# Kernel tuning notes

Measured on AMD Instinct MI355X. Metric: run time of the kernel, lower is better.

Reference implementation:

```python
import jax, jax.numpy as jnp
import numpy as np

N_NODES = 50000
N_EDGES = 800000
D_IN = 128
D_HID = 128
GN_EPS = 1e-5
L2_EPS = 1e-12


def _gcn_conv(x, edge_index, W, b, num_nodes):
    """PyG GCNConv: symmetric normalization with self-loops; x [N, Fin]."""
    src, dst = edge_index[0], edge_index[1]
    loops = jnp.arange(num_nodes, dtype=src.dtype)
    src = jnp.concatenate([src, loops])
    dst = jnp.concatenate([dst, loops])
    ew = jnp.ones(src.shape[0], dtype=x.dtype)
    deg = jax.ops.segment_sum(ew, dst, num_segments=num_nodes)
    dinv = jnp.where(deg > 0, jax.lax.rsqrt(deg), 0.0)
    norm = dinv[src] * dinv[dst]                       # [E+N]
    xw = x @ W                                         # [N, Fout]
    msg = xw[src] * norm[:, None]                      # gather + scale
    out = jax.ops.segment_sum(msg, dst, num_segments=num_nodes)
    return out + b


def _message_norm(x, msg, scale):
    """PyG MessageNorm(learn_scale=True): x + scale * ||x|| * msg/||msg||."""
    msg_n = msg / jnp.maximum(jnp.linalg.norm(msg, axis=-1, keepdims=True), L2_EPS)
    x_norm = jnp.linalg.norm(x, axis=-1, keepdims=True)
    return x + scale * x_norm * msg_n


def _graph_norm(x, weight, bias, mean_scale):
    """PyG GraphNorm, single graph (batch all zeros)."""
    mean = jnp.mean(x, axis=0, keepdims=True)
    out = x - mean * mean_scale
    var = jnp.mean(out * out, axis=0, keepdims=True)
    return weight * out * jax.lax.rsqrt(var + GN_EPS) + bias


def _gelu(x):
    return jax.nn.gelu(x, approximate=False)


def setup_inputs() -> dict:
    key = jax.random.key(0)
    ks = jax.random.split(key, 4)
    X = jax.random.normal(ks[0], (D_IN, N_NODES), dtype=jnp.float32)
    edge_index = jax.random.randint(ks[1], (2, N_EDGES), 0, N_NODES, dtype=jnp.int64)
    W1 = jax.random.normal(ks[2], (D_IN, D_HID), dtype=jnp.float32) * (1.0 / np.sqrt(D_IN))
    b1 = jnp.zeros((D_HID,), dtype=jnp.float32)
    scale1 = jnp.ones((1,), dtype=jnp.float32)
    W2 = jax.random.normal(ks[3], (D_HID, D_IN), dtype=jnp.float32) * (1.0 / np.sqrt(D_HID))
    b2 = jnp.zeros((D_IN,), dtype=jnp.float32)
    scale2 = jnp.ones((1,), dtype=jnp.float32)
    gn_weight = jnp.ones((D_IN,), dtype=jnp.float32)
    gn_bias = jnp.zeros((D_IN,), dtype=jnp.float32)
    gn_mean_scale = jnp.ones((D_IN,), dtype=jnp.float32)
    return {"X": X, "edge_index": edge_index, "W1": W1, "b1": b1, "scale1": scale1,
            "W2": W2, "b2": b2, "scale2": scale2, "gn_weight": gn_weight,
            "gn_bias": gn_bias, "gn_mean_scale": gn_mean_scale}


def reference(X, edge_index, W1, b1, scale1, W2, b2, scale2,
              gn_weight, gn_bias, gn_mean_scale):
    x = X.T                                            # [N, D_IN]
    n = x.shape[0]
    # GCNChain 1
    f = _gelu(_message_norm(x, _gcn_conv(x, edge_index, W1, b1, n), scale1))
    # GCNChain 2
    f = _gelu(_message_norm(f, _gcn_conv(f, edge_index, W2, b2, n), scale2))
    # residual + GraphNorm + GELU
    return _gelu(_graph_norm(f + x, gn_weight, gn_bias, gn_mean_scale))
```

## Files before the change

### kernel.cpp

```cpp
#include <hip/hip_runtime.h>
#include <math.h>

#define D 128
#define CAP 64
#define NBUCK 56
#define BSZ   894
#define CAPB  15360

typedef _Float16 h8 __attribute__((ext_vector_type(8)));
typedef float f4x __attribute__((ext_vector_type(4)));

__device__ __forceinline__ float gelu_f(float v){
    return 0.5f * v * (1.0f + erff(v * 0.70710678f));
}

__global__ void k_init(int* cnt, float* colsum, float* colsq, int* gcur,
                       const float* __restrict__ W1, const float* __restrict__ W2,
                       _Float16* __restrict__ wz1, _Float16* __restrict__ wz2, int N){
    int i = blockIdx.x*blockDim.x + threadIdx.x;
    if (i < N) cnt[i] = 0;
    if (i < D){ colsum[i] = 0.f; colsq[i] = 0.f; }
    if (i < NBUCK) gcur[i] = 0;
    if (i < 32768){
        const float* W = (i < 16384) ? W1 : W2;
        _Float16* wz   = (i < 16384) ? wz1 : wz2;
        int u = i & 16383;
        int jj = u & 7, l = (u>>3)&63, fi = u>>9;
        int kb = fi>>3, j = fi&7;
        int k = kb*32 + (l>>4)*8 + jj;
        int c = j*16 + (l&15);
        wz[u] = (_Float16)W[k*D + c];
    }
}

__global__ __launch_bounds__(256)
void k_part(const int* __restrict__ ei, int* __restrict__ gcur,
            unsigned int* __restrict__ ebin, int E){
    __shared__ int bcnt[NBUCK], bbase[NBUCK], bcur[NBUCK];
    int t = threadIdx.x;
    int chunk = (E + gridDim.x - 1) / gridDim.x;
    int e0 = blockIdx.x*chunk, e1 = min(e0 + chunk, E);
    if (t < NBUCK){ bcnt[t] = 0; bcur[t] = 0; }
    __syncthreads();
    int sl[13], dl[13];
    #pragma unroll
    for (int k = 0; k < 13; k++){
        int e = e0 + t + k*256;
        sl[k] = -1;
        if (e < e1){
            sl[k] = __builtin_nontemporal_load(&ei[e]);
            dl[k] = __builtin_nontemporal_load(&ei[E + e]);
            atomicAdd(&bcnt[dl[k]/BSZ], 1);
        }
    }
    __syncthreads();
    if (t < NBUCK) bbase[t] = atomicAdd(&gcur[t], bcnt[t]);
    __syncthreads();
    #pragma unroll
    for (int k = 0; k < 13; k++){
        if (sl[k] >= 0){
            int d = dl[k], b = d/BSZ;
            int p = atomicAdd(&bcur[b], 1);
            int idx = bbase[b] + p;
            if (idx < CAPB)
                ebin[(size_t)b*CAPB + idx] = ((unsigned)(d - b*BSZ) << 16) | (unsigned)sl[k];
        }
    }
}

__global__ __launch_bounds__(256)
void k_fill2(const unsigned int* __restrict__ ebin, const int* __restrict__ gcur,
             int* cnt, unsigned short* __restrict__ csrc){
    int j = blockIdx.x;
    int x = j & 7, i = j >> 3;
    int b = x*7 + (i % 7);
    int slice = i / 7;
    int cntb = gcur[b]; if (cntb > CAPB) cntb = CAPB;
    int chunk = (cntb + 13) / 14;
    int st = slice*chunk, en = min(st + chunk, cntb);
    const unsigned int* bp = ebin + (size_t)b*CAPB;
    for (int e = st + threadIdx.x; e < en; e += 256){
        unsigned pk = bp[e];
        int s = pk & 0xFFFF;
        int d = b*BSZ + (int)(pk >> 16);
        int p = atomicAdd(&cnt[d], 1);
        if (p < CAP) csrc[(size_t)d*CAP + p] = (unsigned short)s;
    }
}

template<bool TRANS_IN>
__launch_bounds__(256)
__global__ void k_gemm_mfma(const void* __restrict__ inp, const h8* __restrict__ wz,
                            const int* __restrict__ cnt, _Float16* __restrict__ outh,
                            h8* __restrict__ xt16, int N){
    __shared__ _Float16 a_lds[8192];
    int t = threadIdx.x;
    int n0 = blockIdx.x * 64;

    if (TRANS_IN){
        const float* in = (const float*)inp;
        #pragma unroll
        for (int i = 0; i < 32; i++){
            int idx = i*256 + t;
            int k = idx >> 6, nn = idx & 63;
            int n = n0 + nn;
            float v = (n < N) ? in[(size_t)k*N + n] : 0.f;
            int kb = k>>5, ks = k&31;
            int lane = (ks>>3)*16 + (nn&15);
            int w = nn>>4;
            a_lds[((kb*4 + w)*64 + lane)*8 + (ks&7)] = (_Float16)v;
        }
    } else {
        const h8* in = (const h8*)inp;
        #pragma unroll
        for (int i = 0; i < 4; i++){
            int idx8 = i*256 + t;
            int nn = idx8 >> 4, kq = idx8 & 15;
            int n = n0 + nn;
            h8 v = {};
            if (n < N) v = in[(size_t)n*16 + kq];
            int kb = kq>>2, quad = kq&3;
            int lane = quad*16 + (nn&15);
            int w = nn>>4;
            *(h8*)&a_lds[((kb*4 + w)*64 + lane)*8] = v;
        }
    }
    __syncthreads();

    int w = t>>6, l = t&63;
    f4x acc[8];
    #pragma unroll
    for (int j = 0; j < 8; j++) acc[j] = (f4x){0.f, 0.f, 0.f, 0.f};
    #pragma unroll
    for (int kb = 0; kb < 4; kb++){
        h8 a = *(const h8*)&a_lds[((kb*4 + w)*64 + l)*8];
        #pragma unroll
        for (int j = 0; j < 8; j++){
            h8 b = wz[(kb*8 + j)*64 + l];
            acc[j] = __builtin_amdgcn_mfma_f32_16x16x32_f16(a, b, acc[j], 0, 0, 0);
        }
    }

    int quad = l>>4, m = l&15;
    #pragma unroll
    for (int r = 0; r < 4; r++){
        int node = n0 + w*16 + quad*4 + r;
        if (node < N){
            float dv = rsqrtf((float)(cnt[node] + 1));
            #pragma unroll
            for (int j = 0; j < 8; j++)
                outh[(size_t)node*D + j*16 + m] = (_Float16)(acc[j][r] * dv);
        }
    }

    if (TRANS_IN && xt16){
        int node = t>>2, kb = t&3;
        int n = n0 + node;
        if (n < N){
            #pragma unroll
            for (int q = 0; q < 4; q++){
                h8 v = *(const h8*)&a_lds[((kb*4 + (node>>4))*64 + q*16 + (node&15))*8];
                xt16[(size_t)n*16 + kb*4 + q] = v;
            }
        }
    }
}

template<bool FINAL>
__launch_bounds__(256)
__global__ void k_gather(const h8* __restrict__ y, const h8* __restrict__ resid,
                         const h8* __restrict__ xorig,
                         const int* __restrict__ cnt,
                         const unsigned short* __restrict__ csrc,
                         const float* __restrict__ bias,
                         const float* __restrict__ scale,
                         h8* __restrict__ out16, int N){
    int n = blockIdx.x*16 + (threadIdx.x >> 4);
    if (n >= N) return;
    int lane = threadIdx.x & 15;
    h8 a0 = y[(size_t)n*16 + lane];
    h8 a1 = {0,0,0,0,0,0,0,0};
    h8 a2 = {0,0,0,0,0,0,0,0};
    h8 a3 = {0,0,0,0,0,0,0,0};
    int mraw = cnt[n];
    float dv = rsqrtf((float)(mraw + 1));
    int m = (mraw < CAP) ? mraw : CAP;
    const unsigned short* sp = csrc + (size_t)n*CAP;
    int j = 0;
    for (; j + 8 <= m; j += 8){
        int s0 = sp[j+0], s1 = sp[j+1], s2 = sp[j+2], s3 = sp[j+3];
        int s4 = sp[j+4], s5 = sp[j+5], s6 = sp[j+6], s7 = sp[j+7];
        h8 v0 = y[(size_t)s0*16 + lane];
        h8 v1 = y[(size_t)s1*16 + lane];
        h8 v2 = y[(size_t)s2*16 + lane];
        h8 v3 = y[(size_t)s3*16 + lane];
        h8 v4 = y[(size_t)s4*16 + lane];
        h8 v5 = y[(size_t)s5*16 + lane];
        h8 v6 = y[(size_t)s6*16 + lane];
        h8 v7 = y[(size_t)s7*16 + lane];
        a0 += v0; a1 += v1; a2 += v2; a3 += v3;
        a0 += v4; a1 += v5; a2 += v6; a3 += v7;
    }
    for (; j + 4 <= m; j += 4){
        int s0 = sp[j+0], s1 = sp[j+1], s2 = sp[j+2], s3 = sp[j+3];
        h8 v0 = y[(size_t)s0*16 + lane];
        h8 v1 = y[(size_t)s1*16 + lane];
        h8 v2 = y[(size_t)s2*16 + lane];
        h8 v3 = y[(size_t)s3*16 + lane];
        a0 += v0; a1 += v1; a2 += v2; a3 += v3;
    }
    for (; j < m; j++){
        int s0 = sp[j];
        a1 += y[(size_t)s0*16 + lane];
    }
    h8 ah = (a0 + a1) + (a2 + a3);

    const float4* bp = (const float4*)&bias[lane*8];
    float4 b0 = bp[0], b1 = bp[1];
    float c[8];
    float nc = 0.f;
    #pragma unroll
    for (int i = 0; i < 8; i++){
        float bb = (i < 4) ? (&b0.x)[i] : (&b1.x)[i-4];
        c[i] = bb + dv * (float)ah[i];
        nc += c[i]*c[i];
    }
    h8 rv = resid[(size_t)n*16 + lane];
    float r[8];
    float nr = 0.f;
    #pragma unroll
    for (int i = 0; i < 8; i++){ r[i] = (float)rv[i]; nr += r[i]*r[i]; }
    #pragma unroll
    for (int mm = 8; mm > 0; mm >>= 1){
        nc += __shfl_xor(nc, mm, 64);
        nr += __shfl_xor(nr, mm, 64);
    }
    float sc = scale[0] * sqrtf(nr) / fmaxf(sqrtf(nc), 1e-12f);
    h8 o;
    #pragma unroll
    for (int i = 0; i < 8; i++){
        float g = gelu_f(r[i] + sc*c[i]);
        if (FINAL){
            h8 xv = xorig[(size_t)n*16 + lane];
            g += (float)xv[i];
        }
        o[i] = (_Float16)g;
    }
    out16[(size_t)n*16 + lane] = o;
}

__global__ void k_stats(const _Float16* __restrict__ h, float* colsum, float* colsq, int N){
    __shared__ float ls[256], ls2[256];
    int t = threadIdx.x;
    int f = t & 127, half = t >> 7;
    float s = 0.f, s2 = 0.f;
    for (int n = blockIdx.x*2 + half; n < N; n += gridDim.x*2){
        float v = (float)h[(size_t)n*D + f]; s += v; s2 += v*v;
    }
    ls[t] = s; ls2[t] = s2;
    __syncthreads();
    if (t < 128){
        s  = ls[t]  + ls[t+128];
        s2 = ls2[t] + ls2[t+128];
        atomicAdd(&colsum[f], s);
        atomicAdd(&colsq[f], s2);
    }
}

__global__ void k_final(const h8* __restrict__ h16,
                        const float* __restrict__ colsum, const float* __restrict__ colsq,
                        const float* __restrict__ gw, const float* __restrict__ gb,
                        const float* __restrict__ ms,
                        float* __restrict__ outp, int N){
    __shared__ float cf[D], sh[D];
    int t = threadIdx.x;
    if (t < D){
        float invN = 1.0f / (float)N;
        float mean = colsum[t] * invN;
        float c = mean * ms[t];
        float var = colsq[t]*invN - 2.f*c*mean + c*c;
        float a = gw[t] * rsqrtf(var + 1e-5f);
        cf[t] = a;
        sh[t] = gb[t] - c*a;
    }
    __syncthreads();
    int i = blockIdx.x*blockDim.x + t;
    if (i < N*16){
        int n = i >> 4, lane = i & 15;
        h8 v = h16[i];
        int f = lane*8;
        float4 o0, o1;
        o0.x = gelu_f((float)v[0]*cf[f+0] + sh[f+0]);
        o0.y = gelu_f((float)v[1]*cf[f+1] + sh[f+1]);
        o0.z = gelu_f((float)v[2]*cf[f+2] + sh[f+2]);
        o0.w = gelu_f((float)v[3]*cf[f+3] + sh[f+3]);
        o1.x = gelu_f((float)v[4]*cf[f+4] + sh[f+4]);
        o1.y = gelu_f((float)v[5]*cf[f+5] + sh[f+5]);
        o1.z = gelu_f((float)v[6]*cf[f+6] + sh[f+6]);
        o1.w = gelu_f((float)v[7]*cf[f+7] + sh[f+7]);
        *(float4*)&outp[(size_t)n*D + f]     = o0;
        *(float4*)&outp[(size_t)n*D + f + 4] = o1;
    }
}

extern "C" void kernel_launch(void* const* d_in, const int* in_sizes, int n_in,
                              void* d_out, int out_size, void* d_ws, size_t ws_size,
                              hipStream_t stream){
    const float* X   = (const float*)d_in[0];
    const int*   ei  = (const int*)  d_in[1];
    const float* W1  = (const float*)d_in[2];
    const float* b1  = (const float*)d_in[3];
    const float* s1  = (const float*)d_in[4];
    const float* W2  = (const float*)d_in[5];
    const float* b2  = (const float*)d_in[6];
    const float* s2  = (const float*)d_in[7];
    const float* gw  = (const float*)d_in[8];
    const float* gb  = (const float*)d_in[9];
    const float* gms = (const float*)d_in[10];
    int N = in_sizes[0] / D;
    int E = in_sizes[1] / 2;
    float* out = (float*)d_out;

    char* ws = (char*)d_ws;
    size_t o = 0;
    auto alloc = [&](size_t bytes)->void*{
        o = (o + 255) & ~(size_t)255;
        void* p = ws + o; o += bytes; return p;
    };
    int*            cnt    = (int*)           alloc((size_t)N * sizeof(int));
    unsigned short* csrc   = (unsigned short*)alloc((size_t)N * CAP * sizeof(unsigned short));
    unsigned int*   ebin   = (unsigned int*)  alloc((size_t)NBUCK * CAPB * sizeof(unsigned int));
    int*            gcur   = (int*)           alloc(NBUCK * sizeof(int));
    float*          colsum = (float*)         alloc(D * sizeof(float));
    float*          colsq  = (float*)         alloc(D * sizeof(float));
    _Float16*       wz1    = (_Float16*)      alloc(16384 * sizeof(_Float16));
    _Float16*       wz2    = (_Float16*)      alloc(16384 * sizeof(_Float16));
    _Float16*       A      = (_Float16*)      alloc((size_t)N * D * sizeof(_Float16));
    h8*             XT16   = (h8*)            alloc((size_t)N * D * sizeof(_Float16));
    h8*             F1     = (h8*)            alloc((size_t)N * D * sizeof(_Float16));
    h8*             B16    = (h8*)            alloc((size_t)N * D * sizeof(_Float16));

    k_init<<<(N+255)/256, 256, 0, stream>>>(cnt, colsum, colsq, gcur, W1, W2, wz1, wz2, N);
    k_part<<<256, 256, 0, stream>>>(ei, gcur, ebin, E);
    k_fill2<<<784, 256, 0, stream>>>(ebin, gcur, cnt, csrc);

    k_gemm_mfma<true><<<(N+63)/64, 256, 0, stream>>>(X, (const h8*)wz1, cnt, A, XT16, N);
    k_gather<false><<<(N+15)/16, 256, 0, stream>>>((const h8*)A, XT16, (const h8*)nullptr,
                                                   cnt, csrc, b1, s1, F1, N);
    k_gemm_mfma<false><<<(N+63)/64, 256, 0, stream>>>(F1, (const h8*)wz2, cnt, A, (h8*)nullptr, N);
    k_gather<true><<<(N+15)/16, 256, 0, stream>>>((const h8*)A, F1, XT16,
                                                  cnt, csrc, b2, s2, B16, N);
    k_stats<<<256, 256, 0, stream>>>((const _Float16*)B16, colsum, colsq, N);
    k_final<<<(N*16+255)/256, 256, 0, stream>>>(B16, colsum, colsq, gw, gb, gms, out, N);
}
```

Baseline: 276.6 us.

## Build CSR per bucket in LDS and fuse first gather with second GEMM

Destination buckets become power-of-two sized (512 nodes). k_fill2 now builds each bucket's neighbour lists and counts in shared memory, then copies them to global memory in coalesced form. This removes the global atomics on cnt and the separate zeroing of cnt. The first aggregation + MessageNorm + GELU is fused with the second MFMA GEMM, so F1 no longer has to be read back from global memory, and one launch is dropped. In exchange, the fill step runs on only 98 large blocks each using about 66KB of LDS, and the fused gather uses 4x fewer, longer-running blocks, which may hide gather latency less well.

```diff
diff --git a/kernel.cpp b/kernel.cpp
--- a/kernel.cpp
+++ b/kernel.cpp
@@ -3,9 +3,9 @@
 
 #define D 128
 #define CAP 64
-#define NBUCK 56
-#define BSZ   894
-#define CAPB  15360
+#define NBUCK 98
+#define BSZ   512
+#define CAPB  10240
 
 typedef _Float16 h8 __attribute__((ext_vector_type(8)));
 typedef float f4x __attribute__((ext_vector_type(4)));
@@ -14,11 +14,10 @@
     return 0.5f * v * (1.0f + erff(v * 0.70710678f));
 }
 
-__global__ void k_init(int* cnt, float* colsum, float* colsq, int* gcur,
+__global__ void k_init(float* colsum, float* colsq, int* gcur,
                        const float* __restrict__ W1, const float* __restrict__ W2,
-                       _Float16* __restrict__ wz1, _Float16* __restrict__ wz2, int N){
+                       _Float16* __restrict__ wz1, _Float16* __restrict__ wz2){
     int i = blockIdx.x*blockDim.x + threadIdx.x;
-    if (i < N) cnt[i] = 0;
     if (i < D){ colsum[i] = 0.f; colsq[i] = 0.f; }
     if (i < NBUCK) gcur[i] = 0;
     if (i < 32768){
@@ -50,7 +49,7 @@
         if (e < e1){
             sl[k] = __builtin_nontemporal_load(&ei[e]);
             dl[k] = __builtin_nontemporal_load(&ei[E + e]);
-            atomicAdd(&bcnt[dl[k]/BSZ], 1);
+            atomicAdd(&bcnt[dl[k] >> 9], 1);
         }
     }
     __syncthreads();
@@ -59,71 +58,58 @@
     #pragma unroll
     for (int k = 0; k < 13; k++){
         if (sl[k] >= 0){
-            int d = dl[k], b = d/BSZ;
+            int d = dl[k], b = d >> 9;
             int p = atomicAdd(&bcur[b], 1);
             int idx = bbase[b] + p;
             if (idx < CAPB)
-                ebin[(size_t)b*CAPB + idx] = ((unsigned)(d - b*BSZ) << 16) | (unsigned)sl[k];
+                ebin[(size_t)b*CAPB + idx] = ((unsigned)(d & (BSZ-1)) << 16) | (unsigned)sl[k];
         }
     }
 }
 
 __global__ __launch_bounds__(256)
 void k_fill2(const unsigned int* __restrict__ ebin, const int* __restrict__ gcur,
-             int* cnt, unsigned short* __restrict__ csrc){
-    int j = blockIdx.x;
-    int x = j & 7, i = j >> 3;
-    int b = x*7 + (i % 7);
-    int slice = i / 7;
+             int* __restrict__ cnt, unsigned short* __restrict__ csrc, int N){
+    __shared__ unsigned short slab[BSZ*CAP];
+    __shared__ int lcnt[BSZ];
+    int b = blockIdx.x, t = threadIdx.x;
+    for (int i = t; i < BSZ; i += 256) lcnt[i] = 0;
+    __syncthreads();
     int cntb = gcur[b]; if (cntb > CAPB) cntb = CAPB;
-    int chunk = (cntb + 13) / 14;
-    int st = slice*chunk, en = min(st + chunk, cntb);
     const unsigned int* bp = ebin + (size_t)b*CAPB;
-    for (int e = st + threadIdx.x; e < en; e += 256){
-        unsigned pk = bp[e];
-        int s = pk & 0xFFFF;
-        int d = b*BSZ + (int)(pk >> 16);
-        int p = atomicAdd(&cnt[d], 1);
-        if (p < CAP) csrc[(size_t)d*CAP + p] = (unsigned short)s;
-    }
-}
-
-template<bool TRANS_IN>
+    for (int e = t; e < cntb; e += 256){
+        unsigned pk = __builtin_nontemporal_load(&bp[e]);
+        int dl = pk >> 16;
+        int p = atomicAdd(&lcnt[dl], 1);
+        if (p < CAP) slab[dl*CAP + p] = (unsigned short)(pk & 0xFFFF);
+    }
+    __syncthreads();
+    int base = b*BSZ;
+    int nvalid = N - base; if (nvalid > BSZ) nvalid = BSZ; if (nvalid < 0) nvalid = 0;
+    uint4* dst = (uint4*)&csrc[(size_t)base*CAP];
+    const uint4* src = (const uint4*)slab;
+    for (int i = t; i < nvalid*8; i += 256) dst[i] = src[i];
+    for (int i = t; i < nvalid; i += 256) cnt[base + i] = lcnt[i];
+}
+
 __launch_bounds__(256)
-__global__ void k_gemm_mfma(const void* __restrict__ inp, const h8* __restrict__ wz,
+__global__ void k_gemm_mfma(const float* __restrict__ in, const h8* __restrict__ wz,
                             const int* __restrict__ cnt, _Float16* __restrict__ outh,
                             h8* __restrict__ xt16, int N){
     __shared__ _Float16 a_lds[8192];
     int t = threadIdx.x;
     int n0 = blockIdx.x * 64;
 
-    if (TRANS_IN){
-        const float* in = (const float*)inp;
-        #pragma unroll
-        for (int i = 0; i < 32; i++){
-            int idx = i*256 + t;
-            int k = idx >> 6, nn = idx & 63;
-            int n = n0 + nn;
-            float v = (n < N) ? in[(size_t)k*N + n] : 0.f;
-            int kb = k>>5, ks = k&31;
-            int lane = (ks>>3)*16 + (nn&15);
-            int w = nn>>4;
-            a_lds[((kb*4 + w)*64 + lane)*8 + (ks&7)] = (_Float16)v;
-        }
-    } else {
-        const h8* in = (const h8*)inp;
-        #pragma unroll
-        for (int i = 0; i < 4; i++){
-            int idx8 = i*256 + t;
-            int nn = idx8 >> 4, kq = idx8 & 15;
-            int n = n0 + nn;
-            h8 v = {};
-            if (n < N) v = in[(size_t)n*16 + kq];
-            int kb = kq>>2, quad = kq&3;
-            int lane = quad*16 + (nn&15);
-            int w = nn>>4;
-            *(h8*)&a_lds[((kb*4 + w)*64 + lane)*8] = v;
-        }
+    #pragma unroll
+    for (int i = 0; i < 32; i++){
+        int idx = i*256 + t;
+        int k = idx >> 6, nn = idx & 63;
+        int n = n0 + nn;
+        float v = (n < N) ? in[(size_t)k*N + n] : 0.f;
+        int kb = k>>5, ks = k&31;
+        int lane = (ks>>3)*16 + (nn&15);
+        int w = nn>>4;
+        a_lds[((kb*4 + w)*64 + lane)*8 + (ks&7)] = (_Float16)v;
     }
     __syncthreads();
 
@@ -153,7 +139,7 @@
         }
     }
 
-    if (TRANS_IN && xt16){
+    {
         int node = t>>2, kb = t&3;
         int n = n0 + node;
         if (n < N){
@@ -166,22 +152,124 @@
     }
 }
 
-template<bool FINAL>
 __launch_bounds__(256)
-__global__ void k_gather(const h8* __restrict__ y, const h8* __restrict__ resid,
-                         const h8* __restrict__ xorig,
-                         const int* __restrict__ cnt,
-                         const unsigned short* __restrict__ csrc,
-                         const float* __restrict__ bias,
-                         const float* __restrict__ scale,
-                         h8* __restrict__ out16, int N){
+__global__ void k_gath1(const h8* __restrict__ y, const h8* __restrict__ resid,
+                        const int* __restrict__ cnt,
+                        const unsigned short* __restrict__ csrc,
+                        const float* __restrict__ bias, const float* __restrict__ scale,
+                        const h8* __restrict__ wz,
+                        h8* __restrict__ f1out, _Float16* __restrict__ y2out, int N){
+    __shared__ _Float16 a_lds[8192];
+    int t = threadIdx.x;
+    int n0 = blockIdx.x * 64;
+    int g = t >> 4, lane = t & 15;
+    int kb = lane >> 2, q = lane & 3;
+    const float4* bp = (const float4*)&bias[lane*8];
+    float4 b0 = bp[0], b1v = bp[1];
+    float sc0 = scale[0];
+
+    for (int it = 0; it < 4; it++){
+        int n = n0 + it*16 + g;
+        bool valid = (n < N);
+        h8 a0 = {0,0,0,0,0,0,0,0}, a1 = a0, a2 = a0, a3 = a0;
+        int m = 0; float dv = 1.f;
+        if (valid){
+            int mraw = cnt[n];
+            dv = rsqrtf((float)(mraw + 1));
+            m = (mraw < CAP) ? mraw : CAP;
+            a0 = y[(size_t)n*16 + lane];
+        }
+        const unsigned short* sp = csrc + (size_t)n*CAP;
+        int j = 0;
+        for (; j + 8 <= m; j += 8){
+            int s0 = sp[j+0], s1 = sp[j+1], s2 = sp[j+2], s3 = sp[j+3];
+            int s4 = sp[j+4], s5 = sp[j+5], s6 = sp[j+6], s7 = sp[j+7];
+            h8 v0 = y[(size_t)s0*16 + lane];
+            h8 v1 = y[(size_t)s1*16 + lane];
+            h8 v2 = y[(size_t)s2*16 + lane];
+            h8 v3 = y[(size_t)s3*16 + lane];
+            h8 v4 = y[(size_t)s4*16 + lane];
+            h8 v5 = y[(size_t)s5*16 + lane];
+            h8 v6 = y[(size_t)s6*16 + lane];
+            h8 v7 = y[(size_t)s7*16 + lane];
+            a0 += v0; a1 += v1; a2 += v2; a3 += v3;
+            a0 += v4; a1 += v5; a2 += v6; a3 += v7;
+        }
+        for (; j + 4 <= m; j += 4){
+            int s0 = sp[j+0], s1 = sp[j+1], s2 = sp[j+2], s3 = sp[j+3];
+            h8 v0 = y[(size_t)s0*16 + lane];
+            h8 v1 = y[(size_t)s1*16 + lane];
+            h8 v2 = y[(size_t)s2*16 + lane];
+            h8 v3 = y[(size_t)s3*16 + lane];
+            a0 += v0; a1 += v1; a2 += v2; a3 += v3;
+        }
+        for (; j < m; j++) a1 += y[(size_t)sp[j]*16 + lane];
+        h8 ah = (a0 + a1) + (a2 + a3);
+
+        float c[8], r[8];
+        float nc = 0.f, nr = 0.f;
+        h8 rv = {0,0,0,0,0,0,0,0};
+        if (valid) rv = resid[(size_t)n*16 + lane];
+        #pragma unroll
+        for (int i = 0; i < 8; i++){
+            float bb = (i < 4) ? (&b0.x)[i] : (&b1v.x)[i-4];
+            c[i] = bb + dv * (float)ah[i];
+            nc += c[i]*c[i];
+            r[i] = (float)rv[i];
+            nr += r[i]*r[i];
+        }
+        #pragma unroll
+        for (int mm = 8; mm > 0; mm >>= 1){
+            nc += __shfl_xor(nc, mm, 64);
+            nr += __shfl_xor(nr, mm, 64);
+        }
+        float scl = sc0 * sqrtf(nr) / fmaxf(sqrtf(nc), 1e-12f);
+        h8 o;
+        #pragma unroll
+        for (int i = 0; i < 8; i++) o[i] = (_Float16)gelu_f(r[i] + scl*c[i]);
+        if (valid) f1out[(size_t)n*16 + lane] = o;
+        *(h8*)&a_lds[((kb*4 + it)*64 + q*16 + g)*8] = o;
+    }
+    __syncthreads();
+
+    int w = t>>6, l = t&63;
+    f4x acc[8];
+    #pragma unroll
+    for (int j = 0; j < 8; j++) acc[j] = (f4x){0.f, 0.f, 0.f, 0.f};
+    #pragma unroll
+    for (int kb2 = 0; kb2 < 4; kb2++){
+        h8 a = *(const h8*)&a_lds[((kb2*4 + w)*64 + l)*8];
+        #pragma unroll
+        for (int j = 0; j < 8; j++){
+            h8 b = wz[(kb2*8 + j)*64 + l];
+            acc[j] = __builtin_amdgcn_mfma_f32_16x16x32_f16(a, b, acc[j], 0, 0, 0);
+        }
+    }
+    int quad = l>>4, mcol = l&15;
+    #pragma unroll
+    for (int r2 = 0; r2 < 4; r2++){
+        int node = n0 + w*16 + quad*4 + r2;
+        if (node < N){
+            float dv = rsqrtf((float)(cnt[node] + 1));
+            #pragma unroll
+            for (int j = 0; j < 8; j++)
+                y2out[(size_t)node*D + j*16 + mcol] = (_Float16)(acc[j][r2] * dv);
+        }
+    }
+}
+
+__launch_bounds__(256)
+__global__ void k_gather2(const h8* __restrict__ y, const h8* __restrict__ resid,
+                          const h8* __restrict__ xorig,
+                          const int* __restrict__ cnt,
+                          const unsigned short* __restrict__ csrc,
+                          const float* __restrict__ bias, const float* __restrict__ scale,
+                          h8* __restrict__ out16, int N){
     int n = blockIdx.x*16 + (threadIdx.x >> 4);
     if (n >= N) return;
     int lane = threadIdx.x & 15;
     h8 a0 = y[(size_t)n*16 + lane];
-    h8 a1 = {0,0,0,0,0,0,0,0};
-    h8 a2 = {0,0,0,0,0,0,0,0};
-    h8 a3 = {0,0,0,0,0,0,0,0};
+    h8 a1 = {0,0,0,0,0,0,0,0}, a2 = a1, a3 = a1;
     int mraw = cnt[n];
     float dv = rsqrtf((float)(mraw + 1));
     int m = (mraw < CAP) ? mraw : CAP;
@@ -209,43 +297,33 @@
         h8 v3 = y[(size_t)s3*16 + lane];
         a0 += v0; a1 += v1; a2 += v2; a3 += v3;
     }
-    for (; j < m; j++){
-        int s0 = sp[j];
-        a1 += y[(size_t)s0*16 + lane];
-    }
+    for (; j < m; j++) a1 += y[(size_t)sp[j]*16 + lane];
     h8 ah = (a0 + a1) + (a2 + a3);
 
     const float4* bp = (const float4*)&bias[lane*8];
-    float4 b0 = bp[0], b1 = bp[1];
-    float c[8];
-    float nc = 0.f;
+    float4 b0 = bp[0], b1v = bp[1];
+    float c[8], r[8];
+    float nc = 0.f, nr = 0.f;
+    h8 rv = resid[(size_t)n*16 + lane];
     #pragma unroll
     for (int i = 0; i < 8; i++){
-        float bb = (i < 4) ? (&b0.x)[i] : (&b1.x)[i-4];
+        float bb = (i < 4) ? (&b0.x)[i] : (&b1v.x)[i-4];
         c[i] = bb + dv * (float)ah[i];
         nc += c[i]*c[i];
-    }
-    h8 rv = resid[(size_t)n*16 + lane];
-    float r[8];
-    float nr = 0.f;
-    #pragma unroll
-    for (int i = 0; i < 8; i++){ r[i] = (float)rv[i]; nr += r[i]*r[i]; }
+        r[i] = (float)rv[i];
+        nr += r[i]*r[i];
+    }
     #pragma unroll
     for (int mm = 8; mm > 0; mm >>= 1){
         nc += __shfl_xor(nc, mm, 64);
         nr += __shfl_xor(nr, mm, 64);
     }
-    float sc = scale[0] * sqrtf(nr) / fmaxf(sqrtf(nc), 1e-12f);
+    float scl = scale[0] * sqrtf(nr) / fmaxf(sqrtf(nc), 1e-12f);
+    h8 xv = xorig[(size_t)n*16 + lane];
     h8 o;
     #pragma unroll
-    for (int i = 0; i < 8; i++){
-        float g = gelu_f(r[i] + sc*c[i]);
-        if (FINAL){
-            h8 xv = xorig[(size_t)n*16 + lane];
-            g += (float)xv[i];
-        }
-        o[i] = (_Float16)g;
-    }
+    for (int i = 0; i < 8; i++)
+        o[i] = (_Float16)(gelu_f(r[i] + scl*c[i]) + (float)xv[i]);
     out16[(size_t)n*16 + lane] = o;
 }
 
@@ -336,20 +414,20 @@
     _Float16*       wz1    = (_Float16*)      alloc(16384 * sizeof(_Float16));
     _Float16*       wz2    = (_Float16*)      alloc(16384 * sizeof(_Float16));
     _Float16*       A      = (_Float16*)      alloc((size_t)N * D * sizeof(_Float16));
+    _Float16*       A2     = (_Float16*)      alloc((size_t)N * D * sizeof(_Float16));
     h8*             XT16   = (h8*)            alloc((size_t)N * D * sizeof(_Float16));
     h8*             F1     = (h8*)            alloc((size_t)N * D * sizeof(_Float16));
     h8*             B16    = (h8*)            alloc((size_t)N * D * sizeof(_Float16));
 
-    k_init<<<(N+255)/256, 256, 0, stream>>>(cnt, colsum, colsq, gcur, W1, W2, wz1, wz2, N);
+    k_init<<<128, 256, 0, stream>>>(colsum, colsq, gcur, W1, W2, wz1, wz2);
     k_part<<<256, 256, 0, stream>>>(ei, gcur, ebin, E);
-    k_fill2<<<784, 256, 0, stream>>>(ebin, gcur, cnt, csrc);
-
-    k_gemm_mfma<true><<<(N+63)/64, 256, 0, stream>>>(X, (const h8*)wz1, cnt, A, XT16, N);
-    k_gather<false><<<(N+15)/16, 256, 0, stream>>>((const h8*)A, XT16, (const h8*)nullptr,
-                                                   cnt, csrc, b1, s1, F1, N);
-    k_gemm_mfma<false><<<(N+63)/64, 256, 0, stream>>>(F1, (const h8*)wz2, cnt, A, (h8*)nullptr, N);
-    k_gather<true><<<(N+15)/16, 256, 0, stream>>>((const h8*)A, F1, XT16,
-                                                  cnt, csrc, b2, s2, B16, N);
+    k_fill2<<<NBUCK, 256, 0, stream>>>(ebin, gcur, cnt, csrc, N);
+
+    k_gemm_mfma<<<(N+63)/64, 256, 0, stream>>>(X, (const h8*)wz1, cnt, A, XT16, N);
+    k_gath1<<<(N+63)/64, 256, 0, stream>>>((const h8*)A, XT16, cnt, csrc, b1, s1,
+                                           (const h8*)wz2, F1, A2, N);
+    k_gather2<<<(N+15)/16, 256, 0, stream>>>((const h8*)A2, F1, XT16,
+                                             cnt, csrc, b2, s2, B16, N);
     k_stats<<<256, 256, 0, stream>>>((const _Float16*)B16, colsum, colsq, N);
     k_final<<<(N*16+255)/256, 256, 0, stream>>>(B16, colsum, colsq, gw, gb, gms, out, N);
 }
```

Result: faster. 263.9 us (-4.6%).
